# Kernel optimization log

Measured on AMD Instinct MI355X. Metric: run time of the kernel, lower is better.

## Reference

```python
import jax, jax.numpy as jnp
import numpy as np

NQ, NK, D = 8192, 8192, 256
NEG_INF = -1e30


def setup_inputs() -> dict:
    key = jax.random.key(0)
    kK, kV, kQ, kM = jax.random.split(key, 4)
    K = jax.random.normal(kK, (NK, D), dtype=jnp.float32)
    V = jax.random.normal(kV, (NK, D), dtype=jnp.float32)
    Q = jax.random.normal(kQ, (NQ, D), dtype=jnp.float32)
    m = jax.random.randint(kM, (NQ, NK), 0, 2) > 0  # bool mask, True = attend
    return {"K": K, "V": V, "Q": Q, "m": m}


def reference(K, V, Q, m):
    # affinity: scaled dot product with optional mask
    scale = 1.0 / jnp.sqrt(jnp.asarray(D, dtype=Q.dtype))
    QKt = jnp.einsum('qd,kd->qk', Q, K) * scale  # [NQ, NK]
    QKt = jnp.where(m, QKt, NEG_INF)
    # normalization: softmax over keys
    QKt_n = jax.nn.softmax(QKt, axis=-1)
    # weighted sum of values
    return QKt_n @ V  # [NQ, D]
```

## Files before the change

### kernel.cpp

```cpp
#include <hip/hip_runtime.h>
#include <stdint.h>
#include <stddef.h>

#define NQS 8192
#define NKS 8192
#define DS  256

typedef _Float16 half8 __attribute__((ext_vector_type(8)));
typedef float floatx4 __attribute__((ext_vector_type(4)));

#define MFMA_F16(A,B,C) __builtin_amdgcn_mfma_f32_16x16x32_f16(A,B,C,0,0,0)

#define GLOAD_LDS16(gp, lp) \
  __builtin_amdgcn_global_load_lds((const __attribute__((address_space(1))) void*)(gp), \
                                   (__attribute__((address_space(3))) void*)(lp), 16, 0, 0)

__device__ __forceinline__ float red16_sum(float x){
  x += __builtin_bit_cast(float, __builtin_amdgcn_update_dpp(0, __builtin_bit_cast(int, x), 0xB1, 0xF, 0xF, true));
  x += __builtin_bit_cast(float, __builtin_amdgcn_update_dpp(0, __builtin_bit_cast(int, x), 0x4E, 0xF, 0xF, true));
  x += __builtin_bit_cast(float, __builtin_amdgcn_update_dpp(0, __builtin_bit_cast(int, x), 0x141, 0xF, 0xF, true));
  x += __builtin_bit_cast(float, __builtin_amdgcn_update_dpp(0, __builtin_bit_cast(int, x), 0x140, 0xF, 0xF, true));
  return x;
}

__global__ void detect_mask(const uint32_t* __restrict__ M, uint32_t* __restrict__ flag){
  __shared__ uint32_t s[256];
  uint32_t acc = 0;
  for (int i = threadIdx.x; i < 16384; i += 256) acc |= M[i];
  s[threadIdx.x] = acc;
  __syncthreads();
  if (threadIdx.x == 0){
    uint32_t t = 0;
    for (int i = 0; i < 256; i++) t |= s[i];
    *flag = (t > 1u) ? 1u : 0u;
  }
}

__global__ void pack_mask(const uint8_t* __restrict__ M8,
                          const uint32_t* __restrict__ flag,
                          uint32_t* __restrict__ Mp){
  const int tid  = blockIdx.x*256 + threadIdx.x;
  const int lane = threadIdx.x & 63;
  if (*flag){
    size_t t = (size_t)tid;
    const uint4* p = (const uint4*)(M8 + (t << 5));
    uint4 a = p[0], b = p[1];
    uint32_t v[8] = {a.x,a.y,a.z,a.w,b.x,b.y,b.z,b.w};
    uint32_t w = 0;
    #pragma unroll
    for (int j=0;j<8;j++){
      w |= (((v[j]      ) & 0xFFu) ? 1u:0u) << (j*4+0);
      w |= (((v[j] >>  8) & 0xFFu) ? 1u:0u) << (j*4+1);
      w |= (((v[j] >> 16) & 0xFFu) ? 1u:0u) << (j*4+2);
      w |= (((v[j] >> 24)        ) ? 1u:0u) << (j*4+3);
    }
    Mp[t] = w;
  } else {
    const uint4* M32 = (const uint4*)M8;
    #pragma unroll
    for (int it=0; it<8; ++it){
      uint4 v = M32[(size_t)it*2097152 + tid];
      uint32_t x = ((v.x?1u:0u)|(v.y?2u:0u)|(v.z?4u:0u)|(v.w?8u:0u)) << ((lane & 7)*4);
      x |= __shfl_xor(x, 1);
      x |= __shfl_xor(x, 2);
      x |= __shfl_xor(x, 4);
      if ((lane & 7) == 0) Mp[(size_t)it*262144 + (tid >> 3)] = x;
    }
  }
}

__global__ void cvt_k(const float* __restrict__ K, _Float16* __restrict__ Kc){
  int gid = blockIdx.x*256 + threadIdx.x;
  int c4 = gid >> 13, key = gid & 8191;
  const float4* base = (const float4*)(K + (size_t)key*DS + c4*32);
  float4 f[8];
  #pragma unroll
  for (int j=0;j<8;j++) f[j] = base[j];
  #pragma unroll
  for (int cc=0; cc<4; cc++){
    float4 a=f[cc*2], b=f[cc*2+1];
    half8 h = {(_Float16)a.x,(_Float16)a.y,(_Float16)a.z,(_Float16)a.w,
               (_Float16)b.x,(_Float16)b.y,(_Float16)b.z,(_Float16)b.w};
    *(half8*)(Kc + ((size_t)(c4*4+cc)*NKS + key)*8) = h;
  }
}
__global__ void cvt_v(const float* __restrict__ V, _Float16* __restrict__ Vc){
  int gid = blockIdx.x*256 + threadIdx.x;
  int kc = gid >> 8, d = gid & 255;
  half8 h;
  #pragma unroll
  for (int j=0;j<8;j++) h[j] = (_Float16)V[(size_t)(kc*8+j)*DS + d];
  *(half8*)(Vc + (size_t)gid*8) = h;
}

__global__ __launch_bounds__(256, 1) void attn_fwd(
  const float* __restrict__ Qf, const _Float16* __restrict__ Kc,
  const _Float16* __restrict__ Vc, const uint32_t* __restrict__ Mp,
  float* __restrict__ Op, float* __restrict__ Lo)
{
  __shared__ _Float16 Kls[2][16384];
  __shared__ _Float16 Vls[2][16384];
  __shared__ _Float16 Plds[4][32*72];

  const int tid  = threadIdx.x;
  const int w    = tid >> 6;
  const int lane = tid & 63;
  const int quad = lane >> 4;
  const int l15  = lane & 15;
  const int b    = blockIdx.x;
  const int g128 = b >> 2;
  const int kh   = b & 3;
  const int rb   = g128 << 7;
  const int kbase = kh << 11;
  const int rowbase = rb + w*32;

  const float kLog = 0.09016844005556021f;
  const float MFIX = 6.0f;

  half8 qf[2][8];
  #pragma unroll
  for (int mi=0;mi<2;mi++){
    const float* qrow = Qf + (size_t)(rowbase + mi*16 + l15)*DS;
    #pragma unroll
    for (int ks=0;ks<8;ks++){
      const float4* s = (const float4*)(qrow + ks*32 + quad*8);
      float4 x = s[0], y = s[1];
      qf[mi][ks] = (half8){(_Float16)x.x,(_Float16)x.y,(_Float16)x.z,(_Float16)x.w,
                           (_Float16)y.x,(_Float16)y.y,(_Float16)y.z,(_Float16)y.w};
    }
  }

  floatx4 O[2][16];
  #pragma unroll
  for (int mi=0;mi<2;mi++)
    #pragma unroll
    for (int n=0;n<16;n++) O[mi][n] = (floatx4){0.f,0.f,0.f,0.f};
  float lst[2][4] = {{0,0,0,0},{0,0,0,0}};

  _Float16* myP = &Plds[w][0];

  {
    const int k0 = kbase;
    #pragma unroll
    for (int j=0;j<8;j++){
      int c = w*8 + j;
      GLOAD_LDS16(Kc + ((size_t)c*NKS + k0 + lane)*8, &Kls[0][c*512]);
    }
    const _Float16* vg = Vc + (size_t)(k0>>3)*2048;
    #pragma unroll
    for (int j=0;j<8;j++)
      GLOAD_LDS16(vg + (size_t)(w*8+j)*512 + lane*8, &Vls[0][(w*8+j)*512]);
  }
  __syncthreads();

  #pragma unroll 1
  for (int it=0; it<32; ++it){
    const int buf = it & 1;
    const int k0  = kbase + (it << 6);

    if (it < 31){
      const int kn = k0 + 64;
      #pragma unroll
      for (int j=0;j<8;j++){
        int c = w*8 + j;
        GLOAD_LDS16(Kc + ((size_t)c*NKS + kn + lane)*8, &Kls[buf^1][c*512]);
      }
      const _Float16* vg = Vc + (size_t)(kn>>3)*2048;
      #pragma unroll
      for (int j=0;j<8;j++)
        GLOAD_LDS16(vg + (size_t)(w*8+j)*512 + lane*8, &Vls[buf^1][(w*8+j)*512]);
    }

    uint2 mw[2][4];
    #pragma unroll
    for (int mi=0;mi<2;mi++)
      #pragma unroll
      for (int r=0;r<4;r++)
        mw[mi][r] = *(const uint2*)&Mp[(size_t)(rowbase + mi*16 + quad*4 + r)*(NKS/32) + (k0 >> 5)];

    floatx4 Sc[2][4];
    #pragma unroll
    for (int mi=0;mi<2;mi++)
      #pragma unroll
      for (int n=0;n<4;n++) Sc[mi][n] = (floatx4){0,0,0,0};
    #pragma unroll
    for (int ks=0;ks<8;ks++){
      #pragma unroll
      for (int n=0;n<4;n++){
        half8 kb = *(const half8*)&Kls[buf][(ks*4+quad)*512 + (n*16+l15)*8];
        Sc[0][n] = MFMA_F16(qf[0][ks], kb, Sc[0][n]);
        Sc[1][n] = MFMA_F16(qf[1][ks], kb, Sc[1][n]);
      }
    }

    #pragma unroll
    for (int mi=0;mi<2;mi++){
      #pragma unroll
      for (int r=0;r<4;r++){
        const int rowoff = (mi*16 + quad*4 + r)*72;
        const uint32_t w0 = mw[mi][r].x, w1 = mw[mi][r].y;
        #pragma unroll
        for (int n=0;n<4;n++){
          uint32_t wsel = (n < 2) ? w0 : w1;
          uint32_t bit  = (wsel >> ((n & 1)*16 + l15)) & 1u;
          float e = __builtin_amdgcn_exp2f(__builtin_fmaf(Sc[mi][n][r], kLog, -MFIX));
          float p = bit ? e : 0.f;
          lst[mi][r] += p;
          myP[rowoff + n*16 + l15] = (_Float16)p;
        }
      }
    }

    half8 pa[2][2];
    #pragma unroll
    for (int mi=0;mi<2;mi++)
      #pragma unroll
      for (int ks2=0;ks2<2;ks2++)
        pa[mi][ks2] = *(const half8*)(myP + (mi*16 + l15)*72 + ks2*32 + quad*8);

    #pragma unroll
    for (int ks2=0;ks2<2;ks2++){
      #pragma unroll
      for (int n=0;n<16;n++){
        half8 vb = *(const half8*)&Vls[buf][(ks2*4+quad)*2048 + (n*16+l15)*8];
        O[0][n] = MFMA_F16(pa[0][ks2], vb, O[0][n]);
        O[1][n] = MFMA_F16(pa[1][ks2], vb, O[1][n]);
      }
    }

    __syncthreads();
  }

  #pragma unroll
  for (int mi=0;mi<2;mi++){
    #pragma unroll
    for (int r=0;r<4;r++){
      float ls = red16_sum(lst[mi][r]);
      int row = w*32 + mi*16 + quad*4 + r;
      if (l15 == 0) Lo[(size_t)b*128 + row] = ls;
      float* orow = Op + ((size_t)b*128 + row)*256;
      #pragma unroll
      for (int n=0;n<16;n++)
        orow[n*16 + l15] = O[mi][n][r];
    }
  }
}

__global__ void combine4(const float* __restrict__ Op, const float* __restrict__ Lo,
                         float* __restrict__ Out){
  int gid = blockIdx.x*256 + threadIdx.x;
  int row = gid >> 6;
  int c4  = (gid & 63) << 2;
  int g   = row >> 7, r = row & 127;

  float lt = 0.f;
  #pragma unroll
  for (int kh=0;kh<4;kh++) lt += Lo[(size_t)(g*4 + kh)*128 + r];
  float li = 1.0f / lt;

  float4 acc = {0,0,0,0};
  #pragma unroll
  for (int kh=0;kh<4;kh++){
    const float4 o = *(const float4*)(Op + ((size_t)(g*4 + kh)*128 + r)*256 + c4);
    acc.x += o.x; acc.y += o.y; acc.z += o.z; acc.w += o.w;
  }
  acc.x *= li; acc.y *= li; acc.z *= li; acc.w *= li;
  *(float4*)(Out + (size_t)row*DS + c4) = acc;
}

extern "C" void kernel_launch(void* const* d_in, const int* in_sizes, int n_in,
                              void* d_out, int out_size, void* d_ws, size_t ws_size,
                              hipStream_t stream){
  (void)in_sizes; (void)n_in; (void)out_size; (void)ws_size;
  const float*   K = (const float*)d_in[0];
  const float*   V = (const float*)d_in[1];
  const float*   Q = (const float*)d_in[2];
  const uint8_t* M = (const uint8_t*)d_in[3];
  float* Out = (float*)d_out;

  _Float16* Kc = (_Float16*)d_ws;
  _Float16* Vc = Kc + (size_t)NKS*DS;
  uint32_t* Mp = (uint32_t*)(Vc + (size_t)NKS*DS);
  float*    Op = (float*)(Mp + (size_t)NQS*(NKS/32));
  float*    Lo = Op + (size_t)256*128*256;
  uint32_t* flag = (uint32_t*)(Lo + 256*128);

  hipLaunchKernelGGL(detect_mask, dim3(1),    dim3(256), 0, stream, (const uint32_t*)M, flag);
  hipLaunchKernelGGL(pack_mask,   dim3(8192), dim3(256), 0, stream, M, flag, Mp);
  hipLaunchKernelGGL(cvt_k, dim3(256),  dim3(256), 0, stream, K, Kc);
  hipLaunchKernelGGL(cvt_v, dim3(1024), dim3(256), 0, stream, V, Vc);
  hipLaunchKernelGGL(attn_fwd, dim3(256), dim3(256), 0, stream, Q, Kc, Vc, Mp, Op, Lo);
  hipLaunchKernelGGL(combine4, dim3(2048), dim3(256), 0, stream, Op, Lo, Out);
}
```

Baseline: 538.8 us.

## Switch attention to 32x32x16 MFMA with register-resident P and tiled K/V layout

```diff
diff --git a/kernel.cpp b/kernel.cpp
--- a/kernel.cpp
+++ b/kernel.cpp
@@ -7,21 +7,15 @@
 #define DS  256
 
 typedef _Float16 half8 __attribute__((ext_vector_type(8)));
-typedef float floatx4 __attribute__((ext_vector_type(4)));
-
-#define MFMA_F16(A,B,C) __builtin_amdgcn_mfma_f32_16x16x32_f16(A,B,C,0,0,0)
+typedef float floatx16 __attribute__((ext_vector_type(16)));
+
+#define MFMA32(A,B,C) __builtin_amdgcn_mfma_f32_32x32x16_f16(A,B,C,0,0,0)
 
 #define GLOAD_LDS16(gp, lp) \
   __builtin_amdgcn_global_load_lds((const __attribute__((address_space(1))) void*)(gp), \
                                    (__attribute__((address_space(3))) void*)(lp), 16, 0, 0)
 
-__device__ __forceinline__ float red16_sum(float x){
-  x += __builtin_bit_cast(float, __builtin_amdgcn_update_dpp(0, __builtin_bit_cast(int, x), 0xB1, 0xF, 0xF, true));
-  x += __builtin_bit_cast(float, __builtin_amdgcn_update_dpp(0, __builtin_bit_cast(int, x), 0x4E, 0xF, 0xF, true));
-  x += __builtin_bit_cast(float, __builtin_amdgcn_update_dpp(0, __builtin_bit_cast(int, x), 0x141, 0xF, 0xF, true));
-  x += __builtin_bit_cast(float, __builtin_amdgcn_update_dpp(0, __builtin_bit_cast(int, x), 0x140, 0xF, 0xF, true));
-  return x;
-}
+#define TILE_ELEMS 16384
 
 __global__ void detect_mask(const uint32_t* __restrict__ M, uint32_t* __restrict__ flag){
   __shared__ uint32_t s[256];
@@ -38,210 +32,209 @@
 
 __global__ void pack_mask(const uint8_t* __restrict__ M8,
                           const uint32_t* __restrict__ flag,
-                          uint32_t* __restrict__ Mp){
-  const int tid  = blockIdx.x*256 + threadIdx.x;
-  const int lane = threadIdx.x & 63;
-  if (*flag){
-    size_t t = (size_t)tid;
-    const uint4* p = (const uint4*)(M8 + (t << 5));
-    uint4 a = p[0], b = p[1];
-    uint32_t v[8] = {a.x,a.y,a.z,a.w,b.x,b.y,b.z,b.w};
-    uint32_t w = 0;
-    #pragma unroll
-    for (int j=0;j<8;j++){
-      w |= (((v[j]      ) & 0xFFu) ? 1u:0u) << (j*4+0);
-      w |= (((v[j] >>  8) & 0xFFu) ? 1u:0u) << (j*4+1);
-      w |= (((v[j] >> 16) & 0xFFu) ? 1u:0u) << (j*4+2);
-      w |= (((v[j] >> 24)        ) ? 1u:0u) << (j*4+3);
-    }
-    Mp[t] = w;
-  } else {
-    const uint4* M32 = (const uint4*)M8;
-    #pragma unroll
-    for (int it=0; it<8; ++it){
-      uint4 v = M32[(size_t)it*2097152 + tid];
-      uint32_t x = ((v.x?1u:0u)|(v.y?2u:0u)|(v.z?4u:0u)|(v.w?8u:0u)) << ((lane & 7)*4);
-      x |= __shfl_xor(x, 1);
-      x |= __shfl_xor(x, 2);
-      x |= __shfl_xor(x, 4);
-      if ((lane & 7) == 0) Mp[(size_t)it*262144 + (tid >> 3)] = x;
-    }
+                          uint32_t* __restrict__ Mp2){
+  __shared__ uint32_t W[256];
+  const int tid = threadIdx.x;
+  const int rb64 = blockIdx.x * 64;
+  const int r  = tid >> 2;
+  const int ws = tid & 3;
+  const bool by = (*flag != 0u);
+  #pragma unroll 1
+  for (int j = 0; j < 64; ++j){
+    const int w = j*4 + ws;
+    uint32_t word = 0;
+    if (by){
+      const uint4* p = (const uint4*)(M8 + (size_t)(rb64 + r)*8192 + w*32);
+      uint4 a = p[0], b = p[1];
+      uint32_t v[8] = {a.x,a.y,a.z,a.w,b.x,b.y,b.z,b.w};
+      #pragma unroll
+      for (int q=0;q<8;q++){
+        word |= (((v[q]      ) & 0xFFu) ? 1u:0u) << (q*4+0);
+        word |= (((v[q] >>  8) & 0xFFu) ? 1u:0u) << (q*4+1);
+        word |= (((v[q] >> 16) & 0xFFu) ? 1u:0u) << (q*4+2);
+        word |= (((v[q] >> 24)        ) ? 1u:0u) << (q*4+3);
+      }
+    } else {
+      const uint4* p = (const uint4*)M8 + (size_t)(rb64 + r)*2048 + w*8;
+      #pragma unroll
+      for (int q=0;q<8;q++){
+        uint4 v = p[q];
+        word |= (v.x?1u:0u) << (q*4+0);
+        word |= (v.y?1u:0u) << (q*4+1);
+        word |= (v.z?1u:0u) << (q*4+2);
+        word |= (v.w?1u:0u) << (q*4+3);
+      }
+    }
+    W[tid] = word;
+    __syncthreads();
+    const int r2 = tid & 63, w2 = tid >> 6;
+    Mp2[(size_t)(j*4 + w2)*NQS + rb64 + r2] = W[r2*4 + w2];
+    __syncthreads();
   }
 }
 
 __global__ void cvt_k(const float* __restrict__ K, _Float16* __restrict__ Kc){
   int gid = blockIdx.x*256 + threadIdx.x;
-  int c4 = gid >> 13, key = gid & 8191;
-  const float4* base = (const float4*)(K + (size_t)key*DS + c4*32);
-  float4 f[8];
-  #pragma unroll
-  for (int j=0;j<8;j++) f[j] = base[j];
-  #pragma unroll
-  for (int cc=0; cc<4; cc++){
-    float4 a=f[cc*2], b=f[cc*2+1];
-    half8 h = {(_Float16)a.x,(_Float16)a.y,(_Float16)a.z,(_Float16)a.w,
-               (_Float16)b.x,(_Float16)b.y,(_Float16)b.z,(_Float16)b.w};
-    *(half8*)(Kc + ((size_t)(c4*4+cc)*NKS + key)*8) = h;
-  }
+  int key = gid & 8191;
+  int c   = gid >> 13;
+  int kt = c >> 1, t = c & 1;
+  const float4* s = (const float4*)(K + (size_t)key*DS + kt*16 + t*8);
+  float4 x = s[0], y = s[1];
+  half8 h = {(_Float16)x.x,(_Float16)x.y,(_Float16)x.z,(_Float16)x.w,
+             (_Float16)y.x,(_Float16)y.y,(_Float16)y.z,(_Float16)y.w};
+  int tile = key >> 6, mt = (key >> 5) & 1, k32 = key & 31;
+  size_t off = (size_t)tile*TILE_ELEMS + (((mt*16 + kt)*2 + t)*32 + k32)*8;
+  *(half8*)(Kc + off) = h;
 }
 __global__ void cvt_v(const float* __restrict__ V, _Float16* __restrict__ Vc){
   int gid = blockIdx.x*256 + threadIdx.x;
-  int kc = gid >> 8, d = gid & 255;
+  int d32 = gid & 31;
+  int t   = (gid >> 5) & 1;
+  int nt  = (gid >> 6) & 7;
+  int kkt = (gid >> 9) & 3;
+  int tile = gid >> 11;
+  int d = nt*32 + d32;
+  int kb8 = tile*64 + kkt*16 + t*8;
   half8 h;
   #pragma unroll
-  for (int j=0;j<8;j++) h[j] = (_Float16)V[(size_t)(kc*8+j)*DS + d];
+  for (int j=0;j<8;j++) h[j] = (_Float16)V[(size_t)(kb8 + j)*DS + d];
   *(half8*)(Vc + (size_t)gid*8) = h;
 }
 
 __global__ __launch_bounds__(256, 1) void attn_fwd(
   const float* __restrict__ Qf, const _Float16* __restrict__ Kc,
-  const _Float16* __restrict__ Vc, const uint32_t* __restrict__ Mp,
+  const _Float16* __restrict__ Vc, const uint32_t* __restrict__ Mp2,
   float* __restrict__ Op, float* __restrict__ Lo)
 {
   __shared__ _Float16 Kls[2][16384];
   __shared__ _Float16 Vls[2][16384];
-  __shared__ _Float16 Plds[4][32*72];
 
   const int tid  = threadIdx.x;
   const int w    = tid >> 6;
   const int lane = tid & 63;
-  const int quad = lane >> 4;
-  const int l15  = lane & 15;
+  const int q32  = lane & 31;
+  const int t    = lane >> 5;
   const int b    = blockIdx.x;
   const int g128 = b >> 2;
   const int kh   = b & 3;
-  const int rb   = g128 << 7;
-  const int kbase = kh << 11;
-  const int rowbase = rb + w*32;
+  const int rowbase = (g128 << 7) + w*32;
+  const int kbase   = kh << 11;
+  const int tile0   = kbase >> 6;
+  const int kw0     = kbase >> 5;
 
   const float kLog = 0.09016844005556021f;
   const float MFIX = 6.0f;
 
-  half8 qf[2][8];
-  #pragma unroll
-  for (int mi=0;mi<2;mi++){
-    const float* qrow = Qf + (size_t)(rowbase + mi*16 + l15)*DS;
-    #pragma unroll
-    for (int ks=0;ks<8;ks++){
-      const float4* s = (const float4*)(qrow + ks*32 + quad*8);
+  half8 qf[16];
+  {
+    const float* qrow = Qf + (size_t)(rowbase + q32)*DS;
+    #pragma unroll
+    for (int kt=0;kt<16;kt++){
+      const float4* s = (const float4*)(qrow + kt*16 + t*8);
       float4 x = s[0], y = s[1];
-      qf[mi][ks] = (half8){(_Float16)x.x,(_Float16)x.y,(_Float16)x.z,(_Float16)x.w,
-                           (_Float16)y.x,(_Float16)y.y,(_Float16)y.z,(_Float16)y.w};
-    }
-  }
-
-  floatx4 O[2][16];
-  #pragma unroll
-  for (int mi=0;mi<2;mi++)
-    #pragma unroll
-    for (int n=0;n<16;n++) O[mi][n] = (floatx4){0.f,0.f,0.f,0.f};
-  float lst[2][4] = {{0,0,0,0},{0,0,0,0}};
-
-  _Float16* myP = &Plds[w][0];
-
-  {
-    const int k0 = kbase;
-    #pragma unroll
-    for (int j=0;j<8;j++){
-      int c = w*8 + j;
-      GLOAD_LDS16(Kc + ((size_t)c*NKS + k0 + lane)*8, &Kls[0][c*512]);
-    }
-    const _Float16* vg = Vc + (size_t)(k0>>3)*2048;
-    #pragma unroll
-    for (int j=0;j<8;j++)
-      GLOAD_LDS16(vg + (size_t)(w*8+j)*512 + lane*8, &Vls[0][(w*8+j)*512]);
+      qf[kt] = (half8){(_Float16)x.x,(_Float16)x.y,(_Float16)x.z,(_Float16)x.w,
+                       (_Float16)y.x,(_Float16)y.y,(_Float16)y.z,(_Float16)y.w};
+    }
+  }
+
+  floatx16 O[8];
+  #pragma unroll
+  for (int nt=0;nt<8;nt++)
+    #pragma unroll
+    for (int i=0;i<16;i++) O[nt][i] = 0.f;
+  float lsum = 0.f;
+
+  #pragma unroll
+  for (int j=0;j<8;j++){
+    int c = w*8 + j;
+    GLOAD_LDS16(Kc + (size_t)tile0*TILE_ELEMS + c*512 + lane*8, &Kls[0][c*512]);
+    GLOAD_LDS16(Vc + (size_t)tile0*TILE_ELEMS + c*512 + lane*8, &Vls[0][c*512]);
   }
   __syncthreads();
 
   #pragma unroll 1
   for (int it=0; it<32; ++it){
     const int buf = it & 1;
-    const int k0  = kbase + (it << 6);
 
     if (it < 31){
-      const int kn = k0 + 64;
+      const size_t tb = (size_t)(tile0 + it + 1)*TILE_ELEMS;
       #pragma unroll
       for (int j=0;j<8;j++){
         int c = w*8 + j;
-        GLOAD_LDS16(Kc + ((size_t)c*NKS + kn + lane)*8, &Kls[buf^1][c*512]);
-      }
-      const _Float16* vg = Vc + (size_t)(kn>>3)*2048;
-      #pragma unroll
-      for (int j=0;j<8;j++)
-        GLOAD_LDS16(vg + (size_t)(w*8+j)*512 + lane*8, &Vls[buf^1][(w*8+j)*512]);
-    }
-
-    uint2 mw[2][4];
-    #pragma unroll
-    for (int mi=0;mi<2;mi++)
-      #pragma unroll
-      for (int r=0;r<4;r++)
-        mw[mi][r] = *(const uint2*)&Mp[(size_t)(rowbase + mi*16 + quad*4 + r)*(NKS/32) + (k0 >> 5)];
-
-    floatx4 Sc[2][4];
-    #pragma unroll
-    for (int mi=0;mi<2;mi++)
-      #pragma unroll
-      for (int n=0;n<4;n++) Sc[mi][n] = (floatx4){0,0,0,0};
-    #pragma unroll
-    for (int ks=0;ks<8;ks++){
-      #pragma unroll
-      for (int n=0;n<4;n++){
-        half8 kb = *(const half8*)&Kls[buf][(ks*4+quad)*512 + (n*16+l15)*8];
-        Sc[0][n] = MFMA_F16(qf[0][ks], kb, Sc[0][n]);
-        Sc[1][n] = MFMA_F16(qf[1][ks], kb, Sc[1][n]);
-      }
-    }
-
-    #pragma unroll
-    for (int mi=0;mi<2;mi++){
-      #pragma unroll
-      for (int r=0;r<4;r++){
-        const int rowoff = (mi*16 + quad*4 + r)*72;
-        const uint32_t w0 = mw[mi][r].x, w1 = mw[mi][r].y;
+        GLOAD_LDS16(Kc + tb + c*512 + lane*8, &Kls[buf^1][c*512]);
+        GLOAD_LDS16(Vc + tb + c*512 + lane*8, &Vls[buf^1][c*512]);
+      }
+    }
+
+    #pragma unroll
+    for (int mt=0; mt<2; ++mt){
+      const uint32_t mw = Mp2[(size_t)(kw0 + it*2 + mt)*NQS + rowbase + q32];
+
+      floatx16 S0, S1;
+      #pragma unroll
+      for (int i=0;i<16;i++){ S0[i]=0.f; S1[i]=0.f; }
+      #pragma unroll
+      for (int kt=0;kt<8;kt++){
+        half8 kA = *(const half8*)&Kls[buf][(((mt*16+kt)*2 + t)*32 + q32)*8];
+        S0 = MFMA32(kA, qf[kt], S0);
+      }
+      #pragma unroll
+      for (int kt=8;kt<16;kt++){
+        half8 kA = *(const half8*)&Kls[buf][(((mt*16+kt)*2 + t)*32 + q32)*8];
+        S1 = MFMA32(kA, qf[kt], S1);
+      }
+
+      uint32_t pk[4][2];
+      #pragma unroll
+      for (int s=0;s<4;s++){
+        float pv[4];
         #pragma unroll
-        for (int n=0;n<4;n++){
-          uint32_t wsel = (n < 2) ? w0 : w1;
-          uint32_t bit  = (wsel >> ((n & 1)*16 + l15)) & 1u;
-          float e = __builtin_amdgcn_exp2f(__builtin_fmaf(Sc[mi][n][r], kLog, -MFIX));
-          float p = bit ? e : 0.f;
-          lst[mi][r] += p;
-          myP[rowoff + n*16 + l15] = (_Float16)p;
+        for (int rr=0;rr<4;rr++){
+          int i = s*4 + rr;
+          int keybit = rr + 8*s + 4*t;
+          float e = __builtin_amdgcn_exp2f(__builtin_fmaf(S0[i]+S1[i], kLog, -MFIX));
+          float p = ((mw >> keybit) & 1u) ? e : 0.f;
+          lsum += p;
+          pv[rr] = p;
         }
-      }
-    }
-
-    half8 pa[2][2];
-    #pragma unroll
-    for (int mi=0;mi<2;mi++)
-      #pragma unroll
-      for (int ks2=0;ks2<2;ks2++)
-        pa[mi][ks2] = *(const half8*)(myP + (mi*16 + l15)*72 + ks2*32 + quad*8);
-
-    #pragma unroll
-    for (int ks2=0;ks2<2;ks2++){
-      #pragma unroll
-      for (int n=0;n<16;n++){
-        half8 vb = *(const half8*)&Vls[buf][(ks2*4+quad)*2048 + (n*16+l15)*8];
-        O[0][n] = MFMA_F16(pa[0][ks2], vb, O[0][n]);
-        O[1][n] = MFMA_F16(pa[1][ks2], vb, O[1][n]);
+        pk[s][0] = __builtin_bit_cast(uint32_t, __builtin_amdgcn_cvt_pkrtz(pv[0], pv[1]));
+        pk[s][1] = __builtin_bit_cast(uint32_t, __builtin_amdgcn_cvt_pkrtz(pv[2], pv[3]));
+      }
+
+      #pragma unroll
+      for (int kt2=0; kt2<2; ++kt2){
+        const int s_own  = kt2*2 + t;
+        const int s_send = kt2*2 + (t^1);
+        uint32_t r0 = __shfl_xor(__builtin_bit_cast(int, pk[s_send][0]), 32);
+        uint32_t r1 = __shfl_xor(__builtin_bit_cast(int, pk[s_send][1]), 32);
+        uint32_t lo0 = (t==0) ? pk[s_own][0] : r0;
+        uint32_t lo1 = (t==0) ? pk[s_own][1] : r1;
+        uint32_t hi0 = (t==0) ? r0 : pk[s_own][0];
+        uint32_t hi1 = (t==0) ? r1 : pk[s_own][1];
+        uint4 u = {lo0, lo1, hi0, hi1};
+        half8 pa = __builtin_bit_cast(half8, u);
+        const int kkt = mt*2 + kt2;
+        #pragma unroll
+        for (int nt=0;nt<8;nt++){
+          half8 vB = *(const half8*)&Vls[buf][(((kkt*8+nt)*2 + t)*32 + q32)*8];
+          O[nt] = MFMA32(pa, vB, O[nt]);
+        }
       }
     }
 
     __syncthreads();
   }
 
-  #pragma unroll
-  for (int mi=0;mi<2;mi++){
-    #pragma unroll
-    for (int r=0;r<4;r++){
-      float ls = red16_sum(lst[mi][r]);
-      int row = w*32 + mi*16 + quad*4 + r;
-      if (l15 == 0) Lo[(size_t)b*128 + row] = ls;
-      float* orow = Op + ((size_t)b*128 + row)*256;
-      #pragma unroll
-      for (int n=0;n<16;n++)
-        orow[n*16 + l15] = O[mi][n][r];
+  lsum += __builtin_bit_cast(float, __shfl_xor(__builtin_bit_cast(int, lsum), 32));
+  if (t == 0) Lo[(size_t)b*128 + w*32 + q32] = lsum;
+
+  float* ob = Op + ((size_t)b*128 + w*32)*256;
+  #pragma unroll
+  for (int nt=0;nt<8;nt++){
+    #pragma unroll
+    for (int i=0;i<16;i++){
+      int row = (i&3) + 8*(i>>2) + 4*t;
+      ob[(size_t)row*256 + nt*32 + q32] = O[nt][i];
     }
   }
 }
@@ -278,17 +271,17 @@
   const uint8_t* M = (const uint8_t*)d_in[3];
   float* Out = (float*)d_out;
 
-  _Float16* Kc = (_Float16*)d_ws;
-  _Float16* Vc = Kc + (size_t)NKS*DS;
-  uint32_t* Mp = (uint32_t*)(Vc + (size_t)NKS*DS);
-  float*    Op = (float*)(Mp + (size_t)NQS*(NKS/32));
-  float*    Lo = Op + (size_t)256*128*256;
+  _Float16* Kc  = (_Float16*)d_ws;
+  _Float16* Vc  = Kc + (size_t)NKS*DS;
+  uint32_t* Mp2 = (uint32_t*)(Vc + (size_t)NKS*DS);
+  float*    Op  = (float*)(Mp2 + (size_t)256*NQS);
+  float*    Lo  = Op + (size_t)256*128*256;
   uint32_t* flag = (uint32_t*)(Lo + 256*128);
 
   hipLaunchKernelGGL(detect_mask, dim3(1),    dim3(256), 0, stream, (const uint32_t*)M, flag);
-  hipLaunchKernelGGL(pack_mask,   dim3(8192), dim3(256), 0, stream, M, flag, Mp);
-  hipLaunchKernelGGL(cvt_k, dim3(256),  dim3(256), 0, stream, K, Kc);
+  hipLaunchKernelGGL(pack_mask,   dim3(128),  dim3(256), 0, stream, M, flag, Mp2);
+  hipLaunchKernelGGL(cvt_k, dim3(1024), dim3(256), 0, stream, K, Kc);
   hipLaunchKernelGGL(cvt_v, dim3(1024), dim3(256), 0, stream, V, Vc);
-  hipLaunchKernelGGL(attn_fwd, dim3(256), dim3(256), 0, stream, Q, Kc, Vc, Mp, Op, Lo);
+  hipLaunchKernelGGL(attn_fwd, dim3(256), dim3(256), 0, stream, Q, Kc, Vc, Mp2, Op, Lo);
   hipLaunchKernelGGL(combine4, dim3(2048), dim3(256), 0, stream, Op, Lo, Out);
 }
```

New measurement: 573.5 us. +6.5%, slower.
